# Kernel tuning notes

Measured on AMD Instinct MI355X. Metric: run time of the kernel, lower is better.

The kernel has to match this reference:

```python
import jax, jax.numpy as jnp
import numpy as np

IN_CH = 256
NUM_CLASSES = 1
CONF_THR = 0.3
NMS_IOU = 0.2
ANCHOR_SIZES = (32.0, 64.0, 128.0)
ASPECTS = (0.5, 1.0, 2.0)
NUM_ANCHORS = len(ANCHOR_SIZES) * len(ASPECTS)  # 9
K_CAND = 1024   # top-score candidates fed to NMS per image
MAX_DET = 100   # max_output_size in source
BN_EPS = 1e-5


def _anchors():
    a = [[s * r / 224.0, s / r / 224.0] for s in ANCHOR_SIZES for r in ASPECTS]
    return jnp.asarray(a, jnp.float32)  # [A, 2] (w, h)


def _conv(x, w, b, pad):
    y = jax.lax.conv_general_dilated(x, w, (1, 1), [(pad, pad), (pad, pad)],
                                     dimension_numbers=('NCHW', 'OIHW', 'NCHW'))
    return y + b[None, :, None, None]


def _bn(x, g, b, m, v):
    inv = jax.lax.rsqrt(v + BN_EPS)
    return (x - m[None, :, None, None]) * (g * inv)[None, :, None, None] + b[None, :, None, None]


def _corners(b):
    return (b[..., 0] - b[..., 2] / 2, b[..., 1] - b[..., 3] / 2,
            b[..., 0] + b[..., 2] / 2, b[..., 1] + b[..., 3] / 2)


def _iou_one(box, boxes):
    # box: [4] cxcywh, boxes: [K,4] -> iou [K]
    ax1, ay1, ax2, ay2 = _corners(box)
    bx1, by1, bx2, by2 = _corners(boxes)
    iw = jnp.maximum(jnp.minimum(ax2, bx2) - jnp.maximum(ax1, bx1), 0.0)
    ih = jnp.maximum(jnp.minimum(ay2, by2) - jnp.maximum(ay1, by1), 0.0)
    inter = iw * ih
    union = (ax2 - ax1) * (ay2 - ay1) + (bx2 - bx1) * (by2 - by1) - inter
    return inter / (union + 1e-16)


def _nms(boxes, scores):
    # boxes [K,4], scores [K] -> kept boxes padded to [MAX_DET,4]
    s0 = jnp.where(scores > CONF_THR, scores, -1.0)

    def body(i, carry):
        s, out = carry
        j = jnp.argmax(s)
        ok = s[j] > 0.0
        box = boxes[j]
        iou = _iou_one(box, boxes)
        s_new = jnp.where(iou > NMS_IOU, -1.0, s).at[j].set(-1.0)
        s = jnp.where(ok, s_new, s)
        out = out.at[i].set(jnp.where(ok, box, jnp.zeros_like(box)))
        return s, out

    _, out = jax.lax.fori_loop(0, MAX_DET, body,
                               (s0, jnp.zeros((MAX_DET, 4), boxes.dtype)))
    return out


def _forward(features, w1, b1, g1, be1, m1, v1, w2, b2, g2, be2, m2, v2, wo, bo):
    x = jax.nn.relu(_bn(_conv(features, w1, b1, 1), g1, be1, m1, v1))
    x = jax.nn.relu(_bn(_conv(x, w2, b2, 1), g2, be2, m2, v2))
    p = _conv(x, wo, bo, 0)                      # [B, A*(5+C), H, W]
    B, _, H, W = p.shape
    p = p.reshape(B, NUM_ANCHORS, 5 + NUM_CLASSES, H, W).transpose(0, 3, 4, 1, 2)  # [B,H,W,A,5+C]
    obj = jax.nn.sigmoid(p[..., 4])
    anch = _anchors()
    gx = jnp.arange(W, dtype=p.dtype)[None, :, None]
    gy = jnp.arange(H, dtype=p.dtype)[:, None, None]
    px = (jax.nn.sigmoid(p[..., 0]) + gx) / W
    py = (jax.nn.sigmoid(p[..., 1]) + gy) / H
    pw = jnp.exp(p[..., 2]) * anch[:, 0]
    ph = jnp.exp(p[..., 3]) * anch[:, 1]
    boxes = jnp.stack([px, py, pw, ph], -1).reshape(B, -1, 4)
    if NUM_CLASSES > 1:
        scores = obj * jax.nn.sigmoid(p[..., 5:]).max(-1)
    else:
        scores = obj
    scores = scores.reshape(B, -1)

    def per_image(bx, sc):
        top_s, idx = jax.lax.top_k(sc, K_CAND)
        return _nms(bx[idx], top_s)

    return jax.vmap(per_image)(boxes, scores)    # [B, MAX_DET, 4]


def setup_inputs() -> dict:
    key = jax.random.key(0)
    ks = jax.random.split(key, 16)
    B = 32
    c1, c2 = IN_CH // 2, IN_CH // 4
    oc = NUM_ANCHORS * (5 + NUM_CLASSES)
    return {
        'features': jax.random.normal(ks[0], (B, IN_CH, 56, 56), jnp.float32),
        'w1': jax.random.normal(ks[1], (c1, IN_CH, 3, 3), jnp.float32) * 0.02,
        'b1': jax.random.normal(ks[2], (c1,), jnp.float32) * 0.02,
        'g1': 1.0 + 0.1 * jax.random.normal(ks[3], (c1,), jnp.float32),
        'be1': 0.1 * jax.random.normal(ks[4], (c1,), jnp.float32),
        'm1': 0.1 * jax.random.normal(ks[5], (c1,), jnp.float32),
        'v1': jax.random.uniform(ks[6], (c1,), jnp.float32, 0.5, 1.5),
        'w2': jax.random.normal(ks[7], (c2, c1, 3, 3), jnp.float32) * 0.03,
        'b2': jax.random.normal(ks[8], (c2,), jnp.float32) * 0.02,
        'g2': 1.0 + 0.1 * jax.random.normal(ks[9], (c2,), jnp.float32),
        'be2': 0.1 * jax.random.normal(ks[10], (c2,), jnp.float32),
        'm2': 0.1 * jax.random.normal(ks[11], (c2,), jnp.float32),
        'v2': jax.random.uniform(ks[12], (c2,), jnp.float32, 0.5, 1.5),
        'wo': jax.random.normal(ks[13], (oc, c2, 1, 1), jnp.float32) * 0.1,
        'bo': jax.random.normal(ks[14], (oc,), jnp.float32) * 0.05,
    }


def reference(features, w1, b1, g1, be1, m1, v1, w2, b2, g2, be2, m2, v2, wo, bo):
    return _forward(features, w1, b1, g1, be1, m1, v1, w2, b2, g2, be2, m2, v2, wo, bo)
```

## Files before the change

kernel.cpp:

```cpp
#include <hip/hip_runtime.h>
#include <math.h>
#include <stdint.h>

constexpr int BB   = 32;
constexpr int HW   = 3136;
constexpr int C0   = 256, C1 = 128, C2 = 64;
constexpr int NA   = 9;
constexpr int NCAND = HW * NA;
constexpr int KSEL  = 1024;
constexpr int MAXDET = 100;

typedef _Float16 half8 __attribute__((ext_vector_type(8)));
typedef _Float16 half4v __attribute__((ext_vector_type(4)));
typedef float    f32x4  __attribute__((ext_vector_type(4)));
typedef float    f32x16 __attribute__((ext_vector_type(16)));

__device__ __forceinline__ void g2l16(const void* g, void* l) {
    auto gp = reinterpret_cast<const __attribute__((address_space(1))) char*>(
        reinterpret_cast<uintptr_t>(g));
    auto lp = reinterpret_cast<__attribute__((address_space(3))) char*>(
        reinterpret_cast<uintptr_t>(l));
    __builtin_amdgcn_global_load_lds(gp, lp, 16, 0, 0);
}

__global__ void bn_prep(const float* __restrict__ g, const float* __restrict__ be,
                        const float* __restrict__ m, const float* __restrict__ v,
                        const float* __restrict__ cb,
                        float* __restrict__ scl, float* __restrict__ tb, int n) {
    int i = threadIdx.x;
    if (i < n) {
        float inv = 1.f / sqrtf(v[i] + 1e-5f);
        float s = g[i] * inv;
        scl[i] = s;
        tb[i] = be[i] + (cb[i] - m[i]) * s;
    }
}

__global__ void reorder_w6(const float* __restrict__ w, _Float16* __restrict__ wc,
                           int CIN, int COUT) {
    int i = blockIdx.x * 256 + threadIdx.x;
    int K = CIN * 9;
    if (i >= 2 * COUT * K) return;
    int ci  = i & 31;
    int row = (i >> 5) % (2 * COUT);
    int ch  = (i >> 5) / (2 * COUT);
    int pl  = row / COUT;
    int oc  = row - pl * COUT;
    int cg = ch / 9, r = ch - cg * 9;
    int cin = cg * 32 + ci;
    float v = w[oc * K + cin * 9 + r];
    _Float16 h = (_Float16)v;
    wc[i] = pl ? (_Float16)(v - (float)h) : h;
}

__global__ __launch_bounds__(256) void nchw_to_nhwc_split(
    const float* __restrict__ in, _Float16* __restrict__ hi, _Float16* __restrict__ lo)
{
    __shared__ float tile[64 * 68];
    const int pt = blockIdx.x * 64, ct = blockIdx.y * 64, b = blockIdx.z;
    const int t = threadIdx.x;
    const int r0 = t >> 4, cidx = (t & 15) * 4;
#pragma unroll
    for (int rr = 0; rr < 64; rr += 16) {
        int r = rr + r0;
        const float* src = in + ((size_t)(b * 256 + ct + r)) * HW + pt + cidx;
        float4 v = *(const float4*)src;
        float* d = &tile[r * 68 + cidx];
        d[0] = v.x; d[1] = v.y; d[2] = v.z; d[3] = v.w;
    }
    __syncthreads();
    const int p = t >> 2, c0 = (t & 3) * 16;
    size_t obase = ((size_t)(b * HW + pt + p)) * 256 + ct + c0;
    half8 h0, h1, l0, l1;
#pragma unroll
    for (int j = 0; j < 16; ++j) {
        float v = tile[(c0 + j) * 68 + p];
        _Float16 hh = (_Float16)v;
        _Float16 ll = (_Float16)(v - (float)hh);
        if (j < 8) { h0[j] = hh; l0[j] = ll; }
        else       { h1[j - 8] = hh; l1[j - 8] = ll; }
    }
    *(half8*)(hi + obase)     = h0;
    *(half8*)(hi + obase + 8) = h1;
    *(half8*)(lo + obase)     = l0;
    *(half8*)(lo + obase + 8) = l1;
}

template <int CIN, int COUT, int MINW, bool NHWC_OUT>
__global__ __launch_bounds__(256, MINW) void conv3x3_v10(
    const _Float16* __restrict__ xhi,
    const _Float16* __restrict__ xlo,
    const _Float16* __restrict__ wc,
    const _Float16* __restrict__ zbuf,
    const float* __restrict__ scl, const float* __restrict__ tb,
    _Float16* __restrict__ ohi,
    _Float16* __restrict__ olo,
    float* __restrict__ onchw)
{
    constexpr int K       = CIN * 9;
    constexpr int NCH     = K / 32;
    constexpr int WROWS   = 2 * COUT;
    constexpr int CHALVES = WROWS * 32;
    constexpr int WI      = WROWS / 64;
    constexpr int PI      = 2;
    constexpr int WOC     = COUT / 64;

    __shared__ __align__(16) _Float16 SP[128 * 64];
    __shared__ __align__(16) _Float16 SW[WROWS * 32];

    const int bid = blockIdx.x;
    const int swz = (bid & 7) * (gridDim.x >> 3) + (bid >> 3);
    const int b = swz / 25;
    const int pixBase = (swz - b * 25) * 128;
    const int bHW = b * HW;

    const int t = threadIdx.x, l = t & 63, w = t >> 6;

    const int cpix = (l & 7) ^ ((l >> 3) & 7);
    const int ppl = cpix >> 2, pq = cpix & 3;
    const _Float16* xsp = ppl ? xlo : xhi;
    int py[4], px[4];
    const _Float16* pbase[4];
#pragma unroll
    for (int i = 0; i < 4; ++i) {
        int p = w * 32 + i * 8 + (l >> 3);
        int pix = pixBase + p;
        py[i] = pix / 56; px[i] = pix - py[i] * 56;
        pbase[i] = xsp + (size_t)(bHW + pix) * CIN + pq * 8;
    }
    const int cw = (l & 3) ^ ((l >> 3) & 3);
    const _Float16* wbase = wc + ((size_t)(w * (WI * 16) + (l >> 2))) * 32 + cw * 8;

    const int wid = t >> 6;
    const int wp = wid & 1, wo = wid >> 1;
    const int lc = l & 31, lk = l >> 5;

    f32x16 acc[PI][WOC];
#pragma unroll
    for (int pi = 0; pi < PI; ++pi)
#pragma unroll
        for (int oi = 0; oi < WOC; ++oi) acc[pi][oi] = (f32x16)0.f;

    auto stage = [&](int ch) {
        int cg = ch / 9, r = ch - cg * 9;
        int ky = r / 3;
        int dy = ky - 1, dx = (r - ky * 3) - 1;
        int off = (dy * 56 + dx) * CIN + cg * 32;
#pragma unroll
        for (int i = 0; i < 4; ++i) {
            bool v = ((unsigned)(py[i] + dy) < 56u) && ((unsigned)(px[i] + dx) < 56u);
            const void* src = v ? (const void*)(pbase[i] + off) : (const void*)zbuf;
            g2l16(src, (void*)&SP[w * 2048 + i * 512]);
        }
        const _Float16* wsrc = wbase + (size_t)ch * CHALVES;
#pragma unroll
        for (int j = 0; j < WI; ++j)
            g2l16((const void*)(wsrc + j * 512), (void*)&SW[(w * WI + j) * 512]);
    };

    auto compute = [&]() {
#pragma unroll
        for (int ks = 0; ks < 2; ++ks) {
            half8 pb[PI][2];
#pragma unroll
            for (int pi = 0; pi < PI; ++pi) {
                int prw = wp * (PI * 32) + pi * 32 + lc;
                int key = prw & 7;
#pragma unroll
                for (int pl2 = 0; pl2 < 2; ++pl2) {
                    int c = pl2 * 4 + ks * 2 + lk;
                    pb[pi][pl2] = *(const half8*)&SP[prw * 64 + ((c ^ key) << 3)];
                }
            }
            half8 wa[WOC][2];
#pragma unroll
            for (int oi = 0; oi < WOC; ++oi)
#pragma unroll
                for (int pl2 = 0; pl2 < 2; ++pl2) {
                    int row = pl2 * COUT + wo * (WOC * 32) + oi * 32 + lc;
                    int c = ks * 2 + lk;
                    wa[oi][pl2] = *(const half8*)&SW[row * 32 + ((c ^ ((row >> 1) & 3)) << 3)];
                }
#pragma unroll
            for (int pi = 0; pi < PI; ++pi)
#pragma unroll
                for (int oi = 0; oi < WOC; ++oi) {
                    acc[pi][oi] = __builtin_amdgcn_mfma_f32_32x32x16_f16(wa[oi][0], pb[pi][0], acc[pi][oi], 0, 0, 0);
                    acc[pi][oi] = __builtin_amdgcn_mfma_f32_32x32x16_f16(wa[oi][0], pb[pi][1], acc[pi][oi], 0, 0, 0);
                    acc[pi][oi] = __builtin_amdgcn_mfma_f32_32x32x16_f16(wa[oi][1], pb[pi][0], acc[pi][oi], 0, 0, 0);
                }
        }
    };

    for (int ch = 0; ch < NCH; ++ch) {
        stage(ch);
        __syncthreads();
        compute();
        __syncthreads();
    }

#pragma unroll
    for (int pi = 0; pi < PI; ++pi) {
        const int pix = pixBase + wp * (PI * 32) + pi * 32 + lc;
        if (pix < HW) {
#pragma unroll
            for (int oi = 0; oi < WOC; ++oi) {
#pragma unroll
                for (int g = 0; g < 4; ++g) {
                    const int oc0 = wo * (WOC * 32) + oi * 32 + 8 * g + 4 * lk;
                    f32x4 s4 = *(const f32x4*)(scl + oc0);
                    f32x4 t4 = *(const f32x4*)(tb + oc0);
                    if constexpr (NHWC_OUT) {
                        half4v hh, ll;
#pragma unroll
                        for (int m2 = 0; m2 < 4; ++m2) {
                            float val = fmaxf(acc[pi][oi][g * 4 + m2] * s4[m2] + t4[m2], 0.f);
                            _Float16 h = (_Float16)val;
                            hh[m2] = h;
                            ll[m2] = (_Float16)(val - (float)h);
                        }
                        size_t o = ((size_t)(bHW + pix)) * COUT + oc0;
                        *(half4v*)(ohi + o) = hh;
                        *(half4v*)(olo + o) = ll;
                    } else {
#pragma unroll
                        for (int m2 = 0; m2 < 4; ++m2) {
                            float val = fmaxf(acc[pi][oi][g * 4 + m2] * s4[m2] + t4[m2], 0.f);
                            onchw[((size_t)(b * COUT + oc0 + m2)) * HW + pix] = val;
                        }
                    }
                }
            }
        }
    }
}

__global__ __launch_bounds__(256) void conv1x1_decode(
    const float* __restrict__ x2, const float* __restrict__ wo,
    const float* __restrict__ bo,
    float* __restrict__ boxes, float* __restrict__ scores)
{
    __shared__ float ws[64 * 56];
    for (int i = threadIdx.x; i < 54 * 64; i += 256) {
        int oc = i % 54, c = i / 54;
        ws[c * 56 + oc] = wo[oc * 64 + c];
    }
    __syncthreads();

    int u = blockIdx.x * 256 + threadIdx.x;
    int a = u % 9;
    int rest = u / 9;
    int quad = rest % 784;
    int b = rest / 784;
    int pix0 = quad * 4;
    int y = pix0 / 56;
    int x0 = pix0 - y * 56;

    const float* xb = x2 + (size_t)b * 64 * HW + pix0;
    float acc[5][4];
#pragma unroll
    for (int j = 0; j < 5; ++j)
#pragma unroll
        for (int p = 0; p < 4; ++p) acc[j][p] = 0.f;

#pragma unroll 8
    for (int c = 0; c < 64; ++c) {
        float4 xv = *(const float4*)(xb + c * HW);
#pragma unroll
        for (int j = 0; j < 5; ++j) {
            float w = ws[c * 56 + a * 6 + j];
            acc[j][0] += w * xv.x;
            acc[j][1] += w * xv.y;
            acc[j][2] += w * xv.z;
            acc[j][3] += w * xv.w;
        }
    }

    int si = a / 3, ri = a - si * 3;
    float sv = (float)(32 << si);
    float rv = 0.5f * (float)(1 << ri);
    float aw = (sv * rv) / 224.f;
    float ah = (sv / rv) / 224.f;
    float bo0 = bo[a * 6 + 0], bo1 = bo[a * 6 + 1], bo2 = bo[a * 6 + 2];
    float bo3 = bo[a * 6 + 3], bo4 = bo[a * 6 + 4];

#pragma unroll
    for (int p = 0; p < 4; ++p) {
        float p0 = acc[0][p] + bo0;
        float p1 = acc[1][p] + bo1;
        float p2 = acc[2][p] + bo2;
        float p3 = acc[3][p] + bo3;
        float p4 = acc[4][p] + bo4;
        float sx = 1.f / (1.f + expf(-p0));
        float sy = 1.f / (1.f + expf(-p1));
        float pxc = (sx + (float)(x0 + p)) / 56.f;
        float pyc = (sy + (float)y) / 56.f;
        float pw = expf(p2) * aw;
        float ph = expf(p3) * ah;
        float sc = 1.f / (1.f + expf(-p4));
        int n = (y * 56 + x0 + p) * 9 + a;
        float4 bx; bx.x = pxc; bx.y = pyc; bx.z = pw; bx.w = ph;
        *(float4*)&boxes[((size_t)b * NCAND + n) * 4] = bx;
        scores[(size_t)b * NCAND + n] = sc;
    }
}

__device__ __forceinline__ unsigned fkey(float f) {
    unsigned u = __float_as_uint(f);
    return (u & 0x80000000u) ? ~u : (u | 0x80000000u);
}

__global__ __launch_bounds__(1024) void topk_select(
    const float* __restrict__ scores, const float* __restrict__ boxes,
    float* __restrict__ cbox, float* __restrict__ csc, int* __restrict__ cidx)
{
    const int b = blockIdx.x, t = threadIdx.x;
    const float* sp = scores + (size_t)b * NCAND;
    const int lane = t & 63, w = t >> 6;

    __shared__ unsigned hist[256];
    __shared__ unsigned wsum[16];
    __shared__ unsigned s_sel, s_need, s_tot0, s_tot1;

    unsigned prefix = 0, maskSo = 0;
    int need = KSEL;

    for (int round = 0; round < 4; ++round) {
        int shift = 24 - round * 8;
        if (t < 256) hist[t] = 0;
        __syncthreads();
        for (int i = t; i < NCAND; i += 1024) {
            unsigned u = fkey(sp[i]);
            if ((u & maskSo) == prefix) atomicAdd(&hist[(u >> shift) & 255], 1u);
        }
        __syncthreads();
        if (t == 0) {
            int rem = need;
            unsigned sel = 0;
            for (int v = 255; v >= 0; --v) {
                int c = (int)hist[v];
                if (c >= rem) { sel = (unsigned)v; break; }
                rem -= c;
            }
            s_sel = sel; s_need = (unsigned)rem;
        }
        __syncthreads();
        prefix |= (s_sel << shift);
        maskSo |= (0xFFu << shift);
        need = (int)s_need;
        __syncthreads();
    }

    const unsigned cutoff = prefix;
    const unsigned needT = (unsigned)need;
    unsigned outBase = 0, tieBase = 0;
    const unsigned long long mlt = (1ull << lane) - 1ull;

    for (int c0 = 0; c0 < NCAND; c0 += 1024) {
        int i = c0 + t;
        bool valid = i < NCAND;
        float sc = valid ? sp[i] : 0.f;
        unsigned u = valid ? fkey(sc) : 0u;
        bool gt = valid && (u > cutoff);
        bool eq = valid && (u == cutoff);

        unsigned long long balE = __ballot(eq);
        unsigned lpE = (unsigned)__popcll(balE & mlt);
        if (lane == 0) wsum[w] = (unsigned)__popcll(balE);
        __syncthreads();
        if (t == 0) {
            unsigned run = 0;
            for (int k = 0; k < 16; ++k) { unsigned x = wsum[k]; wsum[k] = run; run += x; }
            s_tot1 = run;
        }
        __syncthreads();
        unsigned tieRank = tieBase + wsum[w] + lpE;
        bool take = gt || (eq && tieRank < needT);
        __syncthreads();

        unsigned long long balT = __ballot(take);
        unsigned lpT = (unsigned)__popcll(balT & mlt);
        if (lane == 0) wsum[w] = (unsigned)__popcll(balT);
        __syncthreads();
        if (t == 0) {
            unsigned run = 0;
            for (int k = 0; k < 16; ++k) { unsigned x = wsum[k]; wsum[k] = run; run += x; }
            s_tot0 = run;
        }
        __syncthreads();
        unsigned pos = outBase + wsum[w] + lpT;
        if (take) {
            float4 bx = *(const float4*)&boxes[((size_t)b * NCAND + i) * 4];
            *(float4*)&cbox[((size_t)b * KSEL + pos) * 4] = bx;
            csc[(size_t)b * KSEL + pos] = sc;
            cidx[(size_t)b * KSEL + pos] = i;
        }
        tieBase += s_tot1;
        outBase += s_tot0;
        __syncthreads();
    }
}

__global__ __launch_bounds__(64) void nms_wave(
    const float* __restrict__ cbox, const float* __restrict__ csc,
    const int* __restrict__ cidx, float* __restrict__ out)
{
    const int b = blockIdx.x, l = threadIdx.x;
    float cx[16], cy[16], w_[16], h_[16], s[16];
    int id[16];
#pragma unroll
    for (int j = 0; j < 16; ++j) {
        int ci = (b << 10) + (j << 6) + l;
        float4 bb = *(const float4*)&cbox[(size_t)ci * 4];
        float sc = csc[ci];
        cx[j] = bb.x; cy[j] = bb.y; w_[j] = bb.z; h_[j] = bb.w;
        s[j] = sc > 0.3f ? sc : -1.f;
        id[j] = cidx[ci];
    }
    float* ob = out + (size_t)b * MAXDET * 4;

    for (int it = 0; it < MAXDET; ++it) {
        float bs = s[0]; int bi = id[0];
        float bcx = cx[0], bcy = cy[0], bw = w_[0], bh = h_[0];
#pragma unroll
        for (int j = 1; j < 16; ++j) {
            bool tk = (s[j] > bs) || (s[j] == bs && id[j] < bi);
            if (tk) { bs = s[j]; bi = id[j]; bcx = cx[j]; bcy = cy[j]; bw = w_[j]; bh = h_[j]; }
        }
#pragma unroll
        for (int m2 = 1; m2 < 64; m2 <<= 1) {
            float os = __shfl_xor(bs, m2); int oi = __shfl_xor(bi, m2);
            float ox = __shfl_xor(bcx, m2), oy = __shfl_xor(bcy, m2);
            float ow = __shfl_xor(bw, m2), oh2 = __shfl_xor(bh, m2);
            bool tk = (os > bs) || (os == bs && oi < bi);
            if (tk) { bs = os; bi = oi; bcx = ox; bcy = oy; bw = ow; bh = oh2; }
        }
        if (bs <= 0.f) {
            for (int q = it * 4 + l; q < MAXDET * 4; q += 64) ob[q] = 0.f;
            break;
        }
        if (l == 0) {
            float4 o; o.x = bcx; o.y = bcy; o.z = bw; o.w = bh;
            *(float4*)&ob[it * 4] = o;
        }
        float wx1 = bcx - bw / 2.f, wy1 = bcy - bh / 2.f;
        float wx2 = bcx + bw / 2.f, wy2 = bcy + bh / 2.f;
        float war = (wx2 - wx1) * (wy2 - wy1);
#pragma unroll
        for (int j = 0; j < 16; ++j) {
            float jx1 = cx[j] - w_[j] / 2.f, jy1 = cy[j] - h_[j] / 2.f;
            float jx2 = cx[j] + w_[j] / 2.f, jy2 = cy[j] + h_[j] / 2.f;
            float iw = fminf(wx2, jx2) - fmaxf(wx1, jx1); iw = fmaxf(iw, 0.f);
            float ih = fminf(wy2, jy2) - fmaxf(wy1, jy1); ih = fmaxf(ih, 0.f);
            float inter = iw * ih;
            float jar = (jx2 - jx1) * (jy2 - jy1);
            float uni = war + jar - inter;
            if (inter / (uni + 1e-16f) > 0.2f) s[j] = -1.f;
        }
    }
}

extern "C" void kernel_launch(void* const* d_in, const int* in_sizes, int n_in,
                              void* d_out, int out_size, void* d_ws, size_t ws_size,
                              hipStream_t stream)
{
    const float* features = (const float*)d_in[0];
    const float* w1 = (const float*)d_in[1];
    const float* b1 = (const float*)d_in[2];
    const float* g1 = (const float*)d_in[3];
    const float* be1 = (const float*)d_in[4];
    const float* m1 = (const float*)d_in[5];
    const float* v1 = (const float*)d_in[6];
    const float* w2 = (const float*)d_in[7];
    const float* b2 = (const float*)d_in[8];
    const float* g2 = (const float*)d_in[9];
    const float* be2 = (const float*)d_in[10];
    const float* m2 = (const float*)d_in[11];
    const float* v2 = (const float*)d_in[12];
    const float* wo = (const float*)d_in[13];
    const float* bo = (const float*)d_in[14];

    char* ws = (char*)d_ws;
    size_t off = 0;
    auto alloc = [&](size_t bytes) {
        char* p = ws + off;
        off += (bytes + 255) / 256 * 256;
        return p;
    };

    _Float16* zbuf = (_Float16*)alloc(256);
    _Float16* w1c = (_Float16*)alloc((size_t)2 * C1 * 2304 * 2);
    _Float16* w2c = (_Float16*)alloc((size_t)2 * C2 * 1152 * 2);
    float* scl1 = (float*)alloc(C1 * 4);
    float* tb1  = (float*)alloc(C1 * 4);
    float* scl2 = (float*)alloc(C2 * 4);
    float* tb2  = (float*)alloc(C2 * 4);

    const size_t planeF = (size_t)BB * HW * C0 * 2;
    char* regB = alloc(2 * planeF);
    _Float16* fhi = (_Float16*)regB;
    _Float16* flo = (_Float16*)(regB + planeF);

    const size_t planeX1 = (size_t)BB * HW * C1 * 2;
    char* regC = alloc(2 * planeX1);
    _Float16* x1hi = (_Float16*)regC;
    _Float16* x1lo = (_Float16*)(regC + planeX1);

    float* x2     = (float*)regB;
    float* boxes  = (float*)(regB + 25690112);
    float* scores = (float*)(regB + 25690112 + 14450688);
    float* cbox = (float*)regC;
    float* csc  = (float*)(regC + 524288);
    int*   cidx = (int*)(regC + 524288 + 131072);

    hipMemsetAsync(zbuf, 0, 256, stream);
    bn_prep<<<1, 256, 0, stream>>>(g1, be1, m1, v1, b1, scl1, tb1, C1);
    bn_prep<<<1, 256, 0, stream>>>(g2, be2, m2, v2, b2, scl2, tb2, C2);
    reorder_w6<<<(2 * C1 * 2304 + 255) / 256, 256, 0, stream>>>(w1, w1c, C0, C1);
    reorder_w6<<<(2 * C2 * 1152 + 255) / 256, 256, 0, stream>>>(w2, w2c, C1, C2);

    nchw_to_nhwc_split<<<dim3(49, 4, BB), 256, 0, stream>>>(features, fhi, flo);

    conv3x3_v10<C0, C1, 4, true><<<800, 256, 0, stream>>>(
        fhi, flo, w1c, zbuf, scl1, tb1, x1hi, x1lo, nullptr);
    conv3x3_v10<C1, C2, 4, false><<<800, 256, 0, stream>>>(
        x1hi, x1lo, w2c, zbuf, scl2, tb2, nullptr, nullptr, x2);

    conv1x1_decode<<<(BB * 784 * NA) / 256, 256, 0, stream>>>(x2, wo, bo, boxes, scores);

    topk_select<<<BB, 1024, 0, stream>>>(scores, boxes, cbox, csc, cidx);
    nms_wave<<<BB, 64, 0, stream>>>(cbox, csc, cidx, (float*)d_out);
}
```

Before: 650.1 us.

## Merge BN-prep and weight-reorder launches, drop weight LDS swizzle

The two BN parameter prep kernels become one launch, and the two weight reorder/split kernels become one combined grid, cutting the number of small launches from four to two. Separately, the XOR swizzle on the weight tile's LDS layout is removed in the conv kernel: global-to-LDS loads now use a plain column offset and the MFMA weight reads index LDS linearly. Removing the swizzle saves a little address arithmetic, but the weight reads may now hit more LDS bank conflicts.

After: 646.2 us. Within noise of the previous version (-0.6%).

```diff
diff --git a/kernel.cpp b/kernel.cpp
--- a/kernel.cpp
+++ b/kernel.cpp
@@ -23,24 +23,29 @@
     __builtin_amdgcn_global_load_lds(gp, lp, 16, 0, 0);
 }
 
-__global__ void bn_prep(const float* __restrict__ g, const float* __restrict__ be,
-                        const float* __restrict__ m, const float* __restrict__ v,
-                        const float* __restrict__ cb,
-                        float* __restrict__ scl, float* __restrict__ tb, int n) {
+__global__ void bn_prep2(const float* g1, const float* be1, const float* m1,
+                         const float* v1, const float* cb1,
+                         const float* g2, const float* be2, const float* m2,
+                         const float* v2, const float* cb2,
+                         float* scl1, float* tb1, float* scl2, float* tb2) {
     int i = threadIdx.x;
-    if (i < n) {
-        float inv = 1.f / sqrtf(v[i] + 1e-5f);
-        float s = g[i] * inv;
-        scl[i] = s;
-        tb[i] = be[i] + (cb[i] - m[i]) * s;
-    }
-}
-
-__global__ void reorder_w6(const float* __restrict__ w, _Float16* __restrict__ wc,
-                           int CIN, int COUT) {
-    int i = blockIdx.x * 256 + threadIdx.x;
+    if (i < C1) {
+        float inv = 1.f / sqrtf(v1[i] + 1e-5f);
+        float s = g1[i] * inv;
+        scl1[i] = s;
+        tb1[i] = be1[i] + (cb1[i] - m1[i]) * s;
+    }
+    if (i < C2) {
+        float inv = 1.f / sqrtf(v2[i] + 1e-5f);
+        float s = g2[i] * inv;
+        scl2[i] = s;
+        tb2[i] = be2[i] + (cb2[i] - m2[i]) * s;
+    }
+}
+
+__device__ __forceinline__ void reorder_one(const float* w, _Float16* wc,
+                                            int i, int CIN, int COUT) {
     int K = CIN * 9;
-    if (i >= 2 * COUT * K) return;
     int ci  = i & 31;
     int row = (i >> 5) % (2 * COUT);
     int ch  = (i >> 5) / (2 * COUT);
@@ -53,6 +58,15 @@
     wc[i] = pl ? (_Float16)(v - (float)h) : h;
 }
 
+__global__ void reorder_w_both(const float* __restrict__ w1, _Float16* __restrict__ w1c,
+                               const float* __restrict__ w2, _Float16* __restrict__ w2c) {
+    constexpr int N1 = 2 * C1 * C0 * 9;
+    constexpr int N2 = 2 * C2 * C1 * 9;
+    int i = blockIdx.x * 256 + threadIdx.x;
+    if (i < N1) reorder_one(w1, w1c, i, C0, C1);
+    else if (i < N1 + N2) reorder_one(w2, w2c, i - N1, C1, C2);
+}
+
 __global__ __launch_bounds__(256) void nchw_to_nhwc_split(
     const float* __restrict__ in, _Float16* __restrict__ hi, _Float16* __restrict__ lo)
 {
@@ -87,7 +101,7 @@
 }
 
 template <int CIN, int COUT, int MINW, bool NHWC_OUT>
-__global__ __launch_bounds__(256, MINW) void conv3x3_v10(
+__global__ __launch_bounds__(256, MINW) void conv3x3_v12(
     const _Float16* __restrict__ xhi,
     const _Float16* __restrict__ xlo,
     const _Float16* __restrict__ wc,
@@ -128,8 +142,7 @@
         py[i] = pix / 56; px[i] = pix - py[i] * 56;
         pbase[i] = xsp + (size_t)(bHW + pix) * CIN + pq * 8;
     }
-    const int cw = (l & 3) ^ ((l >> 3) & 3);
-    const _Float16* wbase = wc + ((size_t)(w * (WI * 16) + (l >> 2))) * 32 + cw * 8;
+    const _Float16* wbase = wc + ((size_t)(w * (WI * 16) + (l >> 2))) * 32 + (l & 3) * 8;
 
     const int wid = t >> 6;
     const int wp = wid & 1, wo = wid >> 1;
@@ -179,7 +192,7 @@
                 for (int pl2 = 0; pl2 < 2; ++pl2) {
                     int row = pl2 * COUT + wo * (WOC * 32) + oi * 32 + lc;
                     int c = ks * 2 + lk;
-                    wa[oi][pl2] = *(const half8*)&SW[row * 32 + ((c ^ ((row >> 1) & 3)) << 3)];
+                    wa[oi][pl2] = *(const half8*)&SW[row * 32 + (c << 3)];
                 }
 #pragma unroll
             for (int pi = 0; pi < PI; ++pi)
@@ -514,16 +527,18 @@
     int*   cidx = (int*)(regC + 524288 + 131072);
 
     hipMemsetAsync(zbuf, 0, 256, stream);
-    bn_prep<<<1, 256, 0, stream>>>(g1, be1, m1, v1, b1, scl1, tb1, C1);
-    bn_prep<<<1, 256, 0, stream>>>(g2, be2, m2, v2, b2, scl2, tb2, C2);
-    reorder_w6<<<(2 * C1 * 2304 + 255) / 256, 256, 0, stream>>>(w1, w1c, C0, C1);
-    reorder_w6<<<(2 * C2 * 1152 + 255) / 256, 256, 0, stream>>>(w2, w2c, C1, C2);
+    bn_prep2<<<1, 256, 0, stream>>>(g1, be1, m1, v1, b1, g2, be2, m2, v2, b2,
+                                    scl1, tb1, scl2, tb2);
+    {
+        int total = 2 * C1 * 2304 + 2 * C2 * 1152;
+        reorder_w_both<<<(total + 255) / 256, 256, 0, stream>>>(w1, w1c, w2, w2c);
+    }
 
     nchw_to_nhwc_split<<<dim3(49, 4, BB), 256, 0, stream>>>(features, fhi, flo);
 
-    conv3x3_v10<C0, C1, 4, true><<<800, 256, 0, stream>>>(
+    conv3x3_v12<C0, C1, 4, true><<<800, 256, 0, stream>>>(
         fhi, flo, w1c, zbuf, scl1, tb1, x1hi, x1lo, nullptr);
-    conv3x3_v10<C1, C2, 4, false><<<800, 256, 0, stream>>>(
+    conv3x3_v12<C1, C2, 4, false><<<800, 256, 0, stream>>>(
         x1hi, x1lo, w2c, zbuf, scl2, tb2, nullptr, nullptr, x2);
 
     conv1x1_decode<<<(BB * 784 * NA) / 256, 256, 0, stream>>>(x2, wo, bo, boxes, scores);
```
